# Kernel optimization log

Hardware: AMD Instinct MI355X
Metric: run time of the kernel (lower is better)

## Reference

```python
import jax, jax.numpy as jnp
import numpy as np

D = 256
H = 8
HD = D // H
LN_EPS = 1e-5


def setup_inputs() -> dict:
    key = jax.random.key(0)
    ks = jax.random.split(key, 20)
    N = 768
    s = lambda *sh: 1.0 / np.sqrt(sh[-1])
    inp = {
        "features": jax.random.normal(ks[0], (N, D), jnp.float32),
        "boxes": jax.random.uniform(ks[1], (N, 4), jnp.float32),
        # MultiheadAttention params (torch layout: [out, in])
        "in_proj_w": jax.random.normal(ks[2], (3 * D, D), jnp.float32) * s(D),
        "in_proj_b": jnp.zeros((3 * D,), jnp.float32),
        "out_proj_w": jax.random.normal(ks[3], (D, D), jnp.float32) * s(D),
        "out_proj_b": jnp.zeros((D,), jnp.float32),
        # similarity_net params
        "w1": jax.random.normal(ks[4], (256, 3 * D + 3), jnp.float32) * s(3 * D + 3),
        "b1": jnp.zeros((256,), jnp.float32),
        "ln_g": jnp.ones((256,), jnp.float32),
        "ln_b": jnp.zeros((256,), jnp.float32),
        "w2": jax.random.normal(ks[5], (128, 256), jnp.float32) * s(256),
        "b2": jnp.zeros((128,), jnp.float32),
        "w3": jax.random.normal(ks[6], (64, 128), jnp.float32) * s(128),
        "b3": jnp.zeros((64,), jnp.float32),
        "w4": jax.random.normal(ks[7], (32, 64), jnp.float32) * s(64),
        "b4": jnp.zeros((32,), jnp.float32),
        "w5": jax.random.normal(ks[8], (1, 32), jnp.float32) * s(32),
        "b5": jnp.zeros((1,), jnp.float32),
    }
    return inp


def _mha(x, in_w, in_b, out_w, out_b):
    # x: [N, D]; torch nn.MultiheadAttention self-attention (eval mode)
    N = x.shape[0]
    qkv = x @ in_w.T + in_b                      # [N, 3D]
    q, k, v = jnp.split(qkv, 3, axis=-1)
    q = q.reshape(N, H, HD).transpose(1, 0, 2)   # [H, N, HD]
    k = k.reshape(N, H, HD).transpose(1, 0, 2)
    v = v.reshape(N, H, HD).transpose(1, 0, 2)
    scores = jnp.einsum("hnd,hmd->hnm", q, k) / np.sqrt(HD)
    attn = jax.nn.softmax(scores, axis=-1)
    o = jnp.einsum("hnm,hmd->hnd", attn, v)      # [H, N, HD]
    o = o.transpose(1, 0, 2).reshape(N, D)
    return o @ out_w.T + out_b


def reference(features, boxes, in_proj_w, in_proj_b, out_proj_w, out_proj_b,
              w1, b1, ln_g, ln_b, w2, b2, w3, b3, w4, b4, w5, b5):
    N = features.shape[0]
    att = _mha(features, in_proj_w, in_proj_b, out_proj_w, out_proj_b)  # [N, D]

    fi = jnp.broadcast_to(att[:, None, :], (N, N, D))
    fj = jnp.broadcast_to(att[None, :, :], (N, N, D))
    bi = boxes[:, None, :]
    bj = boxes[None, :, :]
    x_dist = jnp.abs(bi[:, :, 0] - bj[:, :, 0])
    y_diff = bi[:, :, 1] - bj[:, :, 1]
    spatial = jnp.stack([x_dist, jnp.abs(y_diff), y_diff], axis=-1)    # [N, N, 3]
    pairs = jnp.concatenate([fi, fj, fi * fj, spatial], axis=-1)       # [N, N, 3D+3]

    h = jax.nn.relu(pairs @ w1.T + b1)
    mu = jnp.mean(h, axis=-1, keepdims=True)
    var = jnp.var(h, axis=-1, keepdims=True)
    h = (h - mu) / jnp.sqrt(var + LN_EPS) * ln_g + ln_b
    h = jax.nn.relu(h @ w2.T + b2)
    h = jax.nn.relu(h @ w3.T + b3)
    h = jax.nn.relu(h @ w4.T + b4)
    logits = (h @ w5.T + b5)[..., 0]                                   # [N, N]

    eye = jnp.eye(N, dtype=logits.dtype)
    return logits * (1.0 - eye) - 1e9 * eye
```

## Files before the change

### kernel.cpp

```cpp
#include <hip/hip_runtime.h>


typedef __attribute__((ext_vector_type(8))) __bf16 bf16x8;
typedef __attribute__((ext_vector_type(4))) float f32x4;
typedef __attribute__((ext_vector_type(8))) int i32x8;

__device__ __forceinline__ float bf2f(unsigned short u) {
    return __uint_as_float(((unsigned int)u) << 16);
}
__device__ __forceinline__ unsigned short f2bf(float f) {
    union { __bf16 b; unsigned short u; } cv;
    cv.b = (__bf16)f;
    return cv.u;
}
__device__ __forceinline__ unsigned pk2(float lo, float hi) {
    return (unsigned)f2bf(lo) | ((unsigned)f2bf(hi) << 16);
}
__device__ __forceinline__ int pk4_fp8(float a, float b, float c, float d) {
    int w = __builtin_amdgcn_cvt_pk_fp8_f32(a, b, 0, false);
    w = __builtin_amdgcn_cvt_pk_fp8_f32(c, d, w, true);
    return w;
}
__device__ __forceinline__ unsigned char f2fp8(float v) {
    return (unsigned char)(__builtin_amdgcn_cvt_pk_fp8_f32(v, 0.f, 0, false) & 0xff);
}
__device__ __forceinline__ bf16x8 load8f_bf(const float* p) {
    float4 a = *reinterpret_cast<const float4*>(p);
    float4 b = *reinterpret_cast<const float4*>(p + 4);
    union { bf16x8 v; unsigned u[4]; } cv;
    cv.u[0] = pk2(a.x, a.y); cv.u[1] = pk2(a.z, a.w);
    cv.u[2] = pk2(b.x, b.y); cv.u[3] = pk2(b.z, b.w);
    return cv.v;
}
__device__ __forceinline__ i32x8 ld32_lds(const unsigned char* p) {
    union { i32x8 v; uint4 q[2]; } r;
    r.q[0] = *reinterpret_cast<const uint4*>(p);
    r.q[1] = *reinterpret_cast<const uint4*>(p + 16);
    return r.v;
}
#define SC1 0x7F7F7F7F
#define MFMA_MX(a, b, c) __builtin_amdgcn_mfma_scale_f32_16x16x128_f8f6f4( \
        (a), (b), (c), 0, 0, 0, SC1, 0, SC1)

__global__ __launch_bounds__(256) void pack_all(
    const float* __restrict__ features, const float* __restrict__ in_proj_w,
    const float* __restrict__ in_proj_b, const float* __restrict__ out_proj_w,
    const float* __restrict__ w1, const float* __restrict__ w2,
    const float* __restrict__ w3, const float* __restrict__ w4,
    const float* __restrict__ b1, const float* __restrict__ ln_g,
    const float* __restrict__ ln_b, const float* __restrict__ b2,
    const float* __restrict__ out_proj_b,
    unsigned short* __restrict__ qkvb, unsigned short* __restrict__ Vt,
    unsigned short* __restrict__ WcatB,
    unsigned char* __restrict__ w1c_mx, unsigned char* __restrict__ w1t_f8,
    unsigned char* __restrict__ w2g_mx, unsigned char* __restrict__ w3_mx,
    unsigned char* __restrict__ w4_f8,
    float* __restrict__ bias768, float* __restrict__ c1, float* __restrict__ c2)
{
    const int blk = blockIdx.x;
    if (blk < 716) {
        int t = blk * 256 + threadIdx.x;
        if (t < 65536) {
            WcatB[t] = f2bf(out_proj_w[t]);
        } else if (t < 131072) {
            int u = t - 65536;
            int e = u & 31, lane = (u >> 5) & 63, f = u >> 11;
            int mt = f & 15, ks = f >> 4;
            int o = mt * 16 + (lane & 15);
            int k = ks * 128 + ((lane >> 4) & 3) * 32 + e;
            w1c_mx[u] = f2fp8(w1[o * 771 + 512 + k]);
        } else if (t < 139264) {
            int u = t - 131072;
            int e = u & 7, lane = (u >> 3) & 63, f = u >> 9;
            int o = f * 16 + (lane & 15);
            int k = ((lane >> 4) & 3) * 8 + e;
            float v = (k < 3) ? w1[o * 771 + 768 + k] : 0.f;
            w1t_f8[u] = f2fp8(v);
        } else if (t < 172032) {
            int u = t - 139264;
            int e = u & 31, lane = (u >> 5) & 63, f = u >> 11;
            int mt = f & 7, ks = f >> 3;
            int p = mt * 16 + (lane & 15);
            int k = ks * 128 + ((lane >> 4) & 3) * 32 + e;
            w2g_mx[u] = f2fp8(w2[p * 256 + k] * ln_g[k]);
        } else if (t < 180224) {
            int u = t - 172032;
            int e = u & 31, lane = (u >> 5) & 63, f = u >> 11;
            int o = f * 16 + (lane & 15);
            int k = ((lane >> 4) & 3) * 32 + e;
            w3_mx[u] = f2fp8(w3[o * 128 + k]);
        } else if (t < 182272) {
            int u = t - 180224;
            int e = u & 7, lane = (u >> 3) & 63, f = u >> 9;
            int l15 = lane & 15, quad = lane >> 4;
            int ct = f & 1, kc = f >> 1;
            int o = ct * 16 + l15, k = kc * 32 + quad * 8 + e;
            w4_f8[u] = f2fp8(w4[o * 64 + k]);
        } else if (t < 183040) {
            int n = t - 182272;
            if (n < 256) bias768[n] = out_proj_b[n];
            else {
                int m = n - 256;
                float s = 0.f;
                for (int d = 0; d < 256; d += 4) {
                    float4 ob = *reinterpret_cast<const float4*>(&out_proj_b[d]);
                    const float* wr = (m < 256) ? &w1[m * 771 + d]
                                                : &w1[(m - 256) * 771 + 256 + d];
                    float4 w = *reinterpret_cast<const float4*>(wr);
                    s += ob.x * w.x + ob.y * w.y + ob.z * w.z + ob.w * w.w;
                }
                bias768[n] = s + ((m < 256) ? b1[m] : 0.f);
            }
        } else if (t < 183168) {
            int p = t - 183040;
            float s2 = 0.f, s1 = 0.f;
            for (int k = 0; k < 256; k += 4) {
                float4 w = *reinterpret_cast<const float4*>(&w2[p * 256 + k]);
                float4 g = *reinterpret_cast<const float4*>(&ln_g[k]);
                float4 lb = *reinterpret_cast<const float4*>(&ln_b[k]);
                s2 += g.x * w.x + g.y * w.y + g.z * w.z + g.w * w.w;
                s1 += lb.x * w.x + lb.y * w.y + lb.z * w.z + lb.w * w.w;
            }
            c2[p] = s2;
            c1[p] = s1 + b2[p];
        }
    } else if (blk < 1228) {
        const int n = blk - 716, e = threadIdx.x;
        const float* wrow = (n < 256) ? &w1[n * 771] : &w1[(n - 256) * 771 + 256];
        float acc = 0.f;
        for (int d = 0; d < 256; d += 4) {
            float4 w = *reinterpret_cast<const float4*>(&wrow[d]);
            acc += w.x * out_proj_w[(d + 0) * 256 + e];
            acc += w.y * out_proj_w[(d + 1) * 256 + e];
            acc += w.z * out_proj_w[(d + 2) * 256 + e];
            acc += w.w * out_proj_w[(d + 3) * 256 + e];
        }
        WcatB[(256 + n) * 256 + e] = f2bf(acc);
    } else {
        const int q = blk - 1228;
        const int bm = q % 12, bn = q / 12;
        const int wv = threadIdx.x >> 6, lane = threadIdx.x & 63;
        const int l15 = lane & 15, quad = lane >> 4;
        const int row0 = bm * 64 + wv * 16;
        const int col0 = bn * 64;
        f32x4 acc[4] = {};
        for (int kc = 0; kc < 8; ++kc) {
            bf16x8 a = load8f_bf(&features[(row0 + l15) * 256 + kc * 32 + quad * 8]);
#pragma unroll
            for (int ct = 0; ct < 4; ++ct) {
                bf16x8 b = load8f_bf(&in_proj_w[(col0 + ct * 16 + l15) * 256 + kc * 32 + quad * 8]);
                acc[ct] = __builtin_amdgcn_mfma_f32_16x16x32_bf16(a, b, acc[ct], 0, 0, 0);
            }
        }
#pragma unroll
        for (int ct = 0; ct < 4; ++ct)
#pragma unroll
            for (int r = 0; r < 4; ++r) {
                int row = row0 + quad * 4 + r, col = col0 + ct * 16 + l15;
                float v = acc[ct][r] + in_proj_b[col];
                if (col < 512) qkvb[row * 768 + col] = f2bf(v);
                else           Vt[(col - 512) * 768 + row] = f2bf(v);
            }
    }
}

__global__ __launch_bounds__(256) void gemm_attab(
    const unsigned short* __restrict__ A, const unsigned short* __restrict__ W,
    const float* __restrict__ bias, float* __restrict__ att,
    float* __restrict__ AB)
{
    const int wv = threadIdx.x >> 6, lane = threadIdx.x & 63;
    const int l15 = lane & 15, quad = lane >> 4;
    const int row0 = blockIdx.x * 64 + wv * 16;
    const int col0 = blockIdx.y * 64;
    f32x4 acc[4] = {};
    for (int kc = 0; kc < 8; ++kc) {
        bf16x8 a = *reinterpret_cast<const bf16x8*>(&A[(row0 + l15) * 256 + kc * 32 + quad * 8]);
#pragma unroll
        for (int ct = 0; ct < 4; ++ct) {
            bf16x8 b = *reinterpret_cast<const bf16x8*>(&W[(col0 + ct * 16 + l15) * 256 + kc * 32 + quad * 8]);
            acc[ct] = __builtin_amdgcn_mfma_f32_16x16x32_bf16(a, b, acc[ct], 0, 0, 0);
        }
    }
#pragma unroll
    for (int ct = 0; ct < 4; ++ct)
#pragma unroll
        for (int r = 0; r < 4; ++r) {
            int row = row0 + quad * 4 + r, col = col0 + ct * 16 + l15;
            float v = acc[ct][r] + bias[col];
            if (col < 256) att[row * 256 + col] = v;
            else           AB[row * 512 + (col - 256)] = v;
        }
}

#define SP 776

__global__ __launch_bounds__(256) void attn_mfma(
    const unsigned short* __restrict__ qkvb, const unsigned short* __restrict__ Vt,
    unsigned short* __restrict__ Obf)
{
    __shared__ __align__(16) unsigned short smS[32 * SP];
    __shared__ float s_inv[32];
    const int h = blockIdx.x, q0 = blockIdx.y * 32, hb = h * 32;
    const int tid = threadIdx.x, wave = tid >> 6, lane = tid & 63;
    const int l15 = lane & 15, quad = lane >> 4;

    bf16x8 af[2];
#pragma unroll
    for (int mt = 0; mt < 2; ++mt)
        af[mt] = *reinterpret_cast<const bf16x8*>(&qkvb[(q0 + mt * 16 + l15) * 768 + hb + quad * 8]);
#pragma unroll
    for (int ct = 0; ct < 12; ++ct) {
        int n0 = wave * 192 + ct * 16;
        bf16x8 b = *reinterpret_cast<const bf16x8*>(&qkvb[(n0 + l15) * 768 + 256 + hb + quad * 8]);
#pragma unroll
        for (int mt = 0; mt < 2; ++mt) {
            f32x4 c = {};
            c = __builtin_amdgcn_mfma_f32_16x16x32_bf16(af[mt], b, c, 0, 0, 0);
#pragma unroll
            for (int r = 0; r < 4; ++r)
                smS[(mt * 16 + quad * 4 + r) * SP + n0 + l15] =
                    f2bf(c[r] * 0.17677669529663689f);
        }
    }
    __syncthreads();

    {
        const int row = tid >> 3, part = tid & 7;
        unsigned short* rp = &smS[row * SP + part * 96];
        float ls = 0.f;
#pragma unroll
        for (int c8 = 0; c8 < 12; ++c8) {
            uint4 v = *reinterpret_cast<const uint4*>(&rp[c8 * 8]);
            const unsigned short* pe = reinterpret_cast<const unsigned short*>(&v);
            unsigned short o8[8];
#pragma unroll
            for (int e = 0; e < 8; ++e) {
                float ev = __expf(bf2f(pe[e]));
                ls += ev;
                o8[e] = f2bf(ev);
            }
            *reinterpret_cast<uint4*>(&rp[c8 * 8]) = *reinterpret_cast<const uint4*>(o8);
        }
        ls += __shfl_xor(ls, 1, 64);
        ls += __shfl_xor(ls, 2, 64);
        ls += __shfl_xor(ls, 4, 64);
        if (part == 0) s_inv[row] = 1.0f / ls;
    }
    __syncthreads();

    const int row0 = (wave >> 1) * 16, cg = wave & 1;
    f32x4 accp = {};
    for (int kc = 0; kc < 24; ++kc) {
        bf16x8 a = *reinterpret_cast<const bf16x8*>(&smS[(row0 + l15) * SP + kc * 32 + quad * 8]);
        bf16x8 b = *reinterpret_cast<const bf16x8*>(&Vt[(hb + cg * 16 + l15) * 768 + kc * 32 + quad * 8]);
        accp = __builtin_amdgcn_mfma_f32_16x16x32_bf16(a, b, accp, 0, 0, 0);
    }
#pragma unroll
    for (int r = 0; r < 4; ++r) {
        int rloc = row0 + quad * 4 + r;
        Obf[(q0 + rloc) * 256 + hb + cg * 16 + l15] = f2bf(accp[r] * s_inv[rloc]);
    }
}

#define S1 304
#define S2 144
#define S3 72

__global__ __launch_bounds__(256, 4) void pair_mlp(
    const float* __restrict__ att, const float* __restrict__ AB,
    const unsigned char* __restrict__ w1c_mx, const unsigned char* __restrict__ w1t_f8,
    const unsigned char* __restrict__ w2g_mx, const unsigned char* __restrict__ w3_mx,
    const unsigned char* __restrict__ w4_f8,
    const float* __restrict__ boxes,
    const float* __restrict__ c1, const float* __restrict__ c2,
    const float* __restrict__ b3, const float* __restrict__ b4,
    const float* __restrict__ w5, const float* __restrict__ b5,
    float* __restrict__ out)
{
    __shared__ __align__(16) unsigned char smH[64 * S1];
    __shared__ __align__(16) unsigned char smH2[64 * S2];
    __shared__ __align__(16) unsigned char smH3[64 * S3];
    __shared__ float s_psum[64][4], s_pssq[64][4];
    __shared__ float s_mu[64], s_rs[64];
    __shared__ float s_l5[64][2];

    const int i    = blockIdx.x;
    const int j0   = blockIdx.y * 64;
    const int tid  = threadIdx.x;
    const int wave = tid >> 6;
    const int lane = tid & 63;
    const int l15  = lane & 15;
    const int quad = lane >> 4;

    {
        const int g = tid & 63;
        float4 fi4 = *reinterpret_cast<const float4*>(&att[i * 256 + g * 4]);
#pragma unroll 4
        for (int it = 0; it < 16; ++it) {
            int r = (tid >> 6) + it * 4;
            float4 aj = *reinterpret_cast<const float4*>(&att[(j0 + r) * 256 + g * 4]);
            *reinterpret_cast<int*>(&smH[r * S1 + g * 4]) =
                pk4_fp8(aj.x * fi4.x, aj.y * fi4.y, aj.z * fi4.z, aj.w * fi4.w);
        }
    }
    if (tid < 64) {
        int j = j0 + tid;
        float xd = fabsf(boxes[i * 4 + 0] - boxes[j * 4 + 0]);
        float yd = boxes[i * 4 + 1] - boxes[j * 4 + 1];
        *reinterpret_cast<int*>(&smH[tid * S1 + 256]) = pk4_fp8(xd, fabsf(yd), yd, 0.f);
        *reinterpret_cast<int*>(&smH[tid * S1 + 260]) = 0;
        *reinterpret_cast<long long*>(&smH[tid * S1 + 264]) = 0;
        *reinterpret_cast<long long*>(&smH[tid * S1 + 272]) = 0;
        *reinterpret_cast<long long*>(&smH[tid * S1 + 280]) = 0;
    }
    __syncthreads();

    f32x4 acc1[4][4] = {};
#pragma unroll
    for (int ks = 0; ks < 2; ++ks) {
#pragma unroll
        for (int mh = 0; mh < 2; ++mh) {
            i32x8 a0 = *reinterpret_cast<const i32x8*>(&w1c_mx[((ks * 16 + wave * 4 + mh * 2 + 0) * 64 + lane) * 32]);
            i32x8 a1 = *reinterpret_cast<const i32x8*>(&w1c_mx[((ks * 16 + wave * 4 + mh * 2 + 1) * 64 + lane) * 32]);
#pragma unroll
            for (int nt = 0; nt < 4; ++nt) {
                i32x8 b = ld32_lds(&smH[(nt * 16 + l15) * S1 + ks * 128 + quad * 32]);
                acc1[mh * 2 + 0][nt] = MFMA_MX(a0, b, acc1[mh * 2 + 0][nt]);
                acc1[mh * 2 + 1][nt] = MFMA_MX(a1, b, acc1[mh * 2 + 1][nt]);
            }
        }
    }
    {
#pragma unroll
        for (int mh = 0; mh < 2; ++mh) {
            long long a0 = *reinterpret_cast<const long long*>(&w1t_f8[((wave * 4 + mh * 2 + 0) * 64 + lane) * 8]);
            long long a1 = *reinterpret_cast<const long long*>(&w1t_f8[((wave * 4 + mh * 2 + 1) * 64 + lane) * 8]);
#pragma unroll
            for (int nt = 0; nt < 4; ++nt) {
                long long b = *reinterpret_cast<const long long*>(&smH[(nt * 16 + l15) * S1 + 256 + quad * 8]);
                acc1[mh * 2 + 0][nt] = __builtin_amdgcn_mfma_f32_16x16x32_fp8_fp8(a0, b, acc1[mh * 2 + 0][nt], 0, 0, 0);
                acc1[mh * 2 + 1][nt] = __builtin_amdgcn_mfma_f32_16x16x32_fp8_fp8(a1, b, acc1[mh * 2 + 1][nt], 0, 0, 0);
            }
        }
    }

    const int o0 = wave * 64;
    float vsum[4] = {}, vssq[4] = {};
#pragma unroll
    for (int mt = 0; mt < 4; ++mt) {
        int o = o0 + mt * 16 + quad * 4;
        float4 Ai = *reinterpret_cast<const float4*>(&AB[i * 512 + o]);
        float AiA[4] = {Ai.x, Ai.y, Ai.z, Ai.w};
#pragma unroll
        for (int nt = 0; nt < 4; ++nt) {
            int j = nt * 16 + l15;
            float4 Bj = *reinterpret_cast<const float4*>(&AB[(j0 + j) * 512 + 256 + o]);
            float BjA[4] = {Bj.x, Bj.y, Bj.z, Bj.w};
#pragma unroll
            for (int r = 0; r < 4; ++r) {
                float v = fmaxf(acc1[mt][nt][r] + AiA[r] + BjA[r], 0.f);
                acc1[mt][nt][r] = v;
                vsum[nt] += v; vssq[nt] += v * v;
            }
        }
    }
#pragma unroll
    for (int nt = 0; nt < 4; ++nt) {
        vsum[nt] += __shfl_xor(vsum[nt], 16, 64);
        vsum[nt] += __shfl_xor(vsum[nt], 32, 64);
        vssq[nt] += __shfl_xor(vssq[nt], 16, 64);
        vssq[nt] += __shfl_xor(vssq[nt], 32, 64);
    }
    if (quad == 0)
#pragma unroll
        for (int nt = 0; nt < 4; ++nt) {
            s_psum[nt * 16 + l15][wave] = vsum[nt];
            s_pssq[nt * 16 + l15][wave] = vssq[nt];
        }
    __syncthreads();
#pragma unroll
    for (int mt = 0; mt < 4; ++mt) {
        int o = o0 + mt * 16 + quad * 4;
#pragma unroll
        for (int nt = 0; nt < 4; ++nt) {
            int j = nt * 16 + l15;
            *reinterpret_cast<int*>(&smH[j * S1 + o]) =
                pk4_fp8(acc1[mt][nt][0], acc1[mt][nt][1], acc1[mt][nt][2], acc1[mt][nt][3]);
        }
    }
    if (wave == 0) {
        int j = lane;
        float sm = (s_psum[j][0] + s_psum[j][1] + s_psum[j][2] + s_psum[j][3]) * (1.0f / 256.0f);
        float sq = (s_pssq[j][0] + s_pssq[j][1] + s_pssq[j][2] + s_pssq[j][3]) * (1.0f / 256.0f);
        s_mu[j] = sm;
        s_rs[j] = rsqrtf(sq - sm * sm + 1e-5f);
    }
    __syncthreads();

    f32x4 acc2[2][4] = {};
#pragma unroll
    for (int ks = 0; ks < 2; ++ks) {
        i32x8 a0 = *reinterpret_cast<const i32x8*>(&w2g_mx[((ks * 8 + wave * 2 + 0) * 64 + lane) * 32]);
        i32x8 a1 = *reinterpret_cast<const i32x8*>(&w2g_mx[((ks * 8 + wave * 2 + 1) * 64 + lane) * 32]);
#pragma unroll
        for (int nt = 0; nt < 4; ++nt) {
            i32x8 b = ld32_lds(&smH[(nt * 16 + l15) * S1 + ks * 128 + quad * 32]);
            acc2[0][nt] = MFMA_MX(a0, b, acc2[0][nt]);
            acc2[1][nt] = MFMA_MX(a1, b, acc2[1][nt]);
        }
    }
#pragma unroll
    for (int mt = 0; mt < 2; ++mt) {
        int p = wave * 32 + mt * 16 + quad * 4;
        float4 C1 = *reinterpret_cast<const float4*>(&c1[p]);
        float4 C2 = *reinterpret_cast<const float4*>(&c2[p]);
        float C1A[4] = {C1.x, C1.y, C1.z, C1.w};
        float C2A[4] = {C2.x, C2.y, C2.z, C2.w};
#pragma unroll
        for (int nt = 0; nt < 4; ++nt) {
            int j = nt * 16 + l15;
            float mu = s_mu[j], rs = s_rs[j];
            float vv[4];
#pragma unroll
            for (int r = 0; r < 4; ++r)
                vv[r] = fmaxf(rs * (acc2[mt][nt][r] - mu * C2A[r]) + C1A[r], 0.f);
            *reinterpret_cast<int*>(&smH2[j * S2 + p]) = pk4_fp8(vv[0], vv[1], vv[2], vv[3]);
        }
    }
    __syncthreads();

    f32x4 acc3[4] = {};
    {
        i32x8 a = *reinterpret_cast<const i32x8*>(&w3_mx[(wave * 64 + lane) * 32]);
#pragma unroll
        for (int nt = 0; nt < 4; ++nt) {
            i32x8 b = ld32_lds(&smH2[(nt * 16 + l15) * S2 + quad * 32]);
            acc3[nt] = MFMA_MX(a, b, acc3[nt]);
        }
    }
    {
        int q = wave * 16 + quad * 4;
        float4 B3 = *reinterpret_cast<const float4*>(&b3[q]);
        float B3A[4] = {B3.x, B3.y, B3.z, B3.w};
#pragma unroll
        for (int nt = 0; nt < 4; ++nt) {
            int j = nt * 16 + l15;
            float vv[4];
#pragma unroll
            for (int r = 0; r < 4; ++r)
                vv[r] = fmaxf(acc3[nt][r] + B3A[r], 0.f);
            *reinterpret_cast<int*>(&smH3[j * S3 + q]) = pk4_fp8(vv[0], vv[1], vv[2], vv[3]);
        }
    }
    __syncthreads();

    const int mt4 = wave & 1;
    const int jh  = wave >> 1;
    f32x4 acc4[2] = {};
#pragma unroll
    for (int kc = 0; kc < 2; ++kc) {
        long long a = *reinterpret_cast<const long long*>(&w4_f8[((kc * 2 + mt4) * 64 + lane) * 8]);
#pragma unroll
        for (int nt = 0; nt < 2; ++nt) {
            int j = jh * 32 + nt * 16 + l15;
            long long b = *reinterpret_cast<const long long*>(&smH3[j * S3 + kc * 32 + quad * 8]);
            acc4[nt] = __builtin_amdgcn_mfma_f32_16x16x32_fp8_fp8(a, b, acc4[nt], 0, 0, 0);
        }
    }
    {
        int o4 = mt4 * 16 + quad * 4;
        float4 B4 = *reinterpret_cast<const float4*>(&b4[o4]);
        float4 W5 = *reinterpret_cast<const float4*>(&w5[o4]);
        float B4A[4] = {B4.x, B4.y, B4.z, B4.w};
        float W5A[4] = {W5.x, W5.y, W5.z, W5.w};
#pragma unroll
        for (int nt = 0; nt < 2; ++nt) {
            float part = 0.f;
#pragma unroll
            for (int r = 0; r < 4; ++r)
                part += fmaxf(acc4[nt][r] + B4A[r], 0.f) * W5A[r];
            part += __shfl_xor(part, 16, 64);
            part += __shfl_xor(part, 32, 64);
            if (quad == 0)
                s_l5[jh * 32 + nt * 16 + l15][mt4] = part;
        }
    }
    __syncthreads();
    if (tid < 64) {
        int j = j0 + tid;
        float v = s_l5[tid][0] + s_l5[tid][1] + b5[0];
        out[i * 768 + j] = (j == i) ? -1.0e9f : v;
    }
}

extern "C" void kernel_launch(void* const* d_in, const int* in_sizes, int n_in,
                              void* d_out, int out_size, void* d_ws, size_t ws_size,
                              hipStream_t stream)
{
    const float* features   = (const float*)d_in[0];
    const float* boxes      = (const float*)d_in[1];
    const float* in_proj_w  = (const float*)d_in[2];
    const float* in_proj_b  = (const float*)d_in[3];
    const float* out_proj_w = (const float*)d_in[4];
    const float* out_proj_b = (const float*)d_in[5];
    const float* w1  = (const float*)d_in[6];
    const float* b1  = (const float*)d_in[7];
    const float* ln_g = (const float*)d_in[8];
    const float* ln_b = (const float*)d_in[9];
    const float* w2  = (const float*)d_in[10];
    const float* b2  = (const float*)d_in[11];
    const float* w3  = (const float*)d_in[12];
    const float* b3  = (const float*)d_in[13];
    const float* w4  = (const float*)d_in[14];
    const float* b4  = (const float*)d_in[15];
    const float* w5  = (const float*)d_in[16];
    const float* b5  = (const float*)d_in[17];
    float* out = (float*)d_out;

    char* p = (char*)d_ws;
    unsigned short* qkvb  = (unsigned short*)p; p += 768 * 768 * 2;
    unsigned short* Vt    = (unsigned short*)p; p += 256 * 768 * 2;
    unsigned short* Obf   = (unsigned short*)p; p += 768 * 256 * 2;
    unsigned short* WcatB = (unsigned short*)p; p += 196608 * 2;
    float* att = (float*)p; p += 768 * 256 * 4;
    float* AB  = (float*)p; p += 768 * 512 * 4;
    unsigned char* w1c_mx = (unsigned char*)p; p += 65536;
    unsigned char* w1t_f8 = (unsigned char*)p; p += 8192;
    unsigned char* w2g_mx = (unsigned char*)p; p += 32768;
    unsigned char* w3_mx  = (unsigned char*)p; p += 8192;
    unsigned char* w4_f8  = (unsigned char*)p; p += 2048;
    float* bias768 = (float*)p; p += 768 * 4;
    float* c1v     = (float*)p; p += 128 * 4;
    float* c2v     = (float*)p; p += 128 * 4;

    pack_all<<<dim3(1372), dim3(256), 0, stream>>>(features, in_proj_w,
        in_proj_b, out_proj_w, w1, w2, w3, w4, b1, ln_g, ln_b, b2, out_proj_b,
        qkvb, Vt, WcatB, w1c_mx, w1t_f8, w2g_mx, w3_mx, w4_f8,
        bias768, c1v, c2v);
    attn_mfma<<<dim3(8, 24), dim3(256), 0, stream>>>(qkvb, Vt, Obf);
    gemm_attab<<<dim3(12, 12), dim3(256), 0, stream>>>(Obf, WcatB, bias768,
        att, AB);
    pair_mlp<<<dim3(768, 12), dim3(256), 0, stream>>>(att, AB,
        w1c_mx, w1t_f8, w2g_mx, w3_mx, w4_f8, boxes, c1v, c2v,
        b3, b4, w5, b5, out);
}
```

Before: 315.8 us.

## Split pair_mlp work across 8 waves per block instead of 4

Doubles the pair_mlp block to 512 threads and repartitions every layer's MFMA tiles so each wave owns half as many output rows or columns. Layer 1 goes from 4 to 2 m-tiles per wave, layer 2 from 2 to 1, and layers 3 and 4 split over j as well. The aim is to cut per-wave accumulator registers and serial MFMA chains, giving more latency hiding within a block. The cost is lower per-wave reuse of B fragments loaded from LDS, more waves contending at each barrier, and occupancy capped by the new launch bounds.

```diff
diff --git a/kernel.cpp b/kernel.cpp
--- a/kernel.cpp
+++ b/kernel.cpp
@@ -267,7 +267,7 @@
 #define S2 144
 #define S3 72
 
-__global__ __launch_bounds__(256, 4) void pair_mlp(
+__global__ __launch_bounds__(512, 2) void pair_mlp(
     const float* __restrict__ att, const float* __restrict__ AB,
     const unsigned char* __restrict__ w1c_mx, const unsigned char* __restrict__ w1t_f8,
     const unsigned char* __restrict__ w2g_mx, const unsigned char* __restrict__ w3_mx,
@@ -281,7 +281,7 @@
     __shared__ __align__(16) unsigned char smH[64 * S1];
     __shared__ __align__(16) unsigned char smH2[64 * S2];
     __shared__ __align__(16) unsigned char smH3[64 * S3];
-    __shared__ float s_psum[64][4], s_pssq[64][4];
+    __shared__ float s_psum[64][8], s_pssq[64][8];
     __shared__ float s_mu[64], s_rs[64];
     __shared__ float s_l5[64][2];
 
@@ -297,8 +297,8 @@
         const int g = tid & 63;
         float4 fi4 = *reinterpret_cast<const float4*>(&att[i * 256 + g * 4]);
 #pragma unroll 4
-        for (int it = 0; it < 16; ++it) {
-            int r = (tid >> 6) + it * 4;
+        for (int it = 0; it < 8; ++it) {
+            int r = (tid >> 6) + it * 8;
             float4 aj = *reinterpret_cast<const float4*>(&att[(j0 + r) * 256 + g * 4]);
             *reinterpret_cast<int*>(&smH[r * S1 + g * 4]) =
                 pk4_fp8(aj.x * fi4.x, aj.y * fi4.y, aj.z * fi4.z, aj.w * fi4.w);
@@ -316,39 +316,33 @@
     }
     __syncthreads();
 
-    f32x4 acc1[4][4] = {};
+    f32x4 acc1[2][4] = {};
 #pragma unroll
     for (int ks = 0; ks < 2; ++ks) {
-#pragma unroll
-        for (int mh = 0; mh < 2; ++mh) {
-            i32x8 a0 = *reinterpret_cast<const i32x8*>(&w1c_mx[((ks * 16 + wave * 4 + mh * 2 + 0) * 64 + lane) * 32]);
-            i32x8 a1 = *reinterpret_cast<const i32x8*>(&w1c_mx[((ks * 16 + wave * 4 + mh * 2 + 1) * 64 + lane) * 32]);
-#pragma unroll
-            for (int nt = 0; nt < 4; ++nt) {
-                i32x8 b = ld32_lds(&smH[(nt * 16 + l15) * S1 + ks * 128 + quad * 32]);
-                acc1[mh * 2 + 0][nt] = MFMA_MX(a0, b, acc1[mh * 2 + 0][nt]);
-                acc1[mh * 2 + 1][nt] = MFMA_MX(a1, b, acc1[mh * 2 + 1][nt]);
-            }
-        }
-    }
-    {
-#pragma unroll
-        for (int mh = 0; mh < 2; ++mh) {
-            long long a0 = *reinterpret_cast<const long long*>(&w1t_f8[((wave * 4 + mh * 2 + 0) * 64 + lane) * 8]);
-            long long a1 = *reinterpret_cast<const long long*>(&w1t_f8[((wave * 4 + mh * 2 + 1) * 64 + lane) * 8]);
-#pragma unroll
-            for (int nt = 0; nt < 4; ++nt) {
-                long long b = *reinterpret_cast<const long long*>(&smH[(nt * 16 + l15) * S1 + 256 + quad * 8]);
-                acc1[mh * 2 + 0][nt] = __builtin_amdgcn_mfma_f32_16x16x32_fp8_fp8(a0, b, acc1[mh * 2 + 0][nt], 0, 0, 0);
-                acc1[mh * 2 + 1][nt] = __builtin_amdgcn_mfma_f32_16x16x32_fp8_fp8(a1, b, acc1[mh * 2 + 1][nt], 0, 0, 0);
-            }
-        }
-    }
-
-    const int o0 = wave * 64;
+        i32x8 a0 = *reinterpret_cast<const i32x8*>(&w1c_mx[((ks * 16 + wave * 2 + 0) * 64 + lane) * 32]);
+        i32x8 a1 = *reinterpret_cast<const i32x8*>(&w1c_mx[((ks * 16 + wave * 2 + 1) * 64 + lane) * 32]);
+#pragma unroll
+        for (int nt = 0; nt < 4; ++nt) {
+            i32x8 b = ld32_lds(&smH[(nt * 16 + l15) * S1 + ks * 128 + quad * 32]);
+            acc1[0][nt] = MFMA_MX(a0, b, acc1[0][nt]);
+            acc1[1][nt] = MFMA_MX(a1, b, acc1[1][nt]);
+        }
+    }
+    {
+        long long a0 = *reinterpret_cast<const long long*>(&w1t_f8[((wave * 2 + 0) * 64 + lane) * 8]);
+        long long a1 = *reinterpret_cast<const long long*>(&w1t_f8[((wave * 2 + 1) * 64 + lane) * 8]);
+#pragma unroll
+        for (int nt = 0; nt < 4; ++nt) {
+            long long b = *reinterpret_cast<const long long*>(&smH[(nt * 16 + l15) * S1 + 256 + quad * 8]);
+            acc1[0][nt] = __builtin_amdgcn_mfma_f32_16x16x32_fp8_fp8(a0, b, acc1[0][nt], 0, 0, 0);
+            acc1[1][nt] = __builtin_amdgcn_mfma_f32_16x16x32_fp8_fp8(a1, b, acc1[1][nt], 0, 0, 0);
+        }
+    }
+
+    const int o0 = wave * 32;
     float vsum[4] = {}, vssq[4] = {};
 #pragma unroll
-    for (int mt = 0; mt < 4; ++mt) {
+    for (int mt = 0; mt < 2; ++mt) {
         int o = o0 + mt * 16 + quad * 4;
         float4 Ai = *reinterpret_cast<const float4*>(&AB[i * 512 + o]);
         float AiA[4] = {Ai.x, Ai.y, Ai.z, Ai.w};
@@ -380,7 +374,7 @@
         }
     __syncthreads();
 #pragma unroll
-    for (int mt = 0; mt < 4; ++mt) {
+    for (int mt = 0; mt < 2; ++mt) {
         int o = o0 + mt * 16 + quad * 4;
 #pragma unroll
         for (int nt = 0; nt < 4; ++nt) {
@@ -391,28 +385,27 @@
     }
     if (wave == 0) {
         int j = lane;
-        float sm = (s_psum[j][0] + s_psum[j][1] + s_psum[j][2] + s_psum[j][3]) * (1.0f / 256.0f);
-        float sq = (s_pssq[j][0] + s_pssq[j][1] + s_pssq[j][2] + s_pssq[j][3]) * (1.0f / 256.0f);
+        float sm = 0.f, sq = 0.f;
+#pragma unroll
+        for (int w = 0; w < 8; ++w) { sm += s_psum[j][w]; sq += s_pssq[j][w]; }
+        sm *= (1.0f / 256.0f); sq *= (1.0f / 256.0f);
         s_mu[j] = sm;
         s_rs[j] = rsqrtf(sq - sm * sm + 1e-5f);
     }
     __syncthreads();
 
-    f32x4 acc2[2][4] = {};
+    f32x4 acc2[4] = {};
 #pragma unroll
     for (int ks = 0; ks < 2; ++ks) {
-        i32x8 a0 = *reinterpret_cast<const i32x8*>(&w2g_mx[((ks * 8 + wave * 2 + 0) * 64 + lane) * 32]);
-        i32x8 a1 = *reinterpret_cast<const i32x8*>(&w2g_mx[((ks * 8 + wave * 2 + 1) * 64 + lane) * 32]);
+        i32x8 a = *reinterpret_cast<const i32x8*>(&w2g_mx[((ks * 8 + wave) * 64 + lane) * 32]);
 #pragma unroll
         for (int nt = 0; nt < 4; ++nt) {
             i32x8 b = ld32_lds(&smH[(nt * 16 + l15) * S1 + ks * 128 + quad * 32]);
-            acc2[0][nt] = MFMA_MX(a0, b, acc2[0][nt]);
-            acc2[1][nt] = MFMA_MX(a1, b, acc2[1][nt]);
-        }
-    }
-#pragma unroll
-    for (int mt = 0; mt < 2; ++mt) {
-        int p = wave * 32 + mt * 16 + quad * 4;
+            acc2[nt] = MFMA_MX(a, b, acc2[nt]);
+        }
+    }
+    {
+        int p = wave * 16 + quad * 4;
         float4 C1 = *reinterpret_cast<const float4*>(&c1[p]);
         float4 C2 = *reinterpret_cast<const float4*>(&c2[p]);
         float C1A[4] = {C1.x, C1.y, C1.z, C1.w};
@@ -424,49 +417,49 @@
             float vv[4];
 #pragma unroll
             for (int r = 0; r < 4; ++r)
-                vv[r] = fmaxf(rs * (acc2[mt][nt][r] - mu * C2A[r]) + C1A[r], 0.f);
+                vv[r] = fmaxf(rs * (acc2[nt][r] - mu * C2A[r]) + C1A[r], 0.f);
             *reinterpret_cast<int*>(&smH2[j * S2 + p]) = pk4_fp8(vv[0], vv[1], vv[2], vv[3]);
         }
     }
     __syncthreads();
 
-    f32x4 acc3[4] = {};
-    {
-        i32x8 a = *reinterpret_cast<const i32x8*>(&w3_mx[(wave * 64 + lane) * 32]);
-#pragma unroll
-        for (int nt = 0; nt < 4; ++nt) {
-            i32x8 b = ld32_lds(&smH2[(nt * 16 + l15) * S2 + quad * 32]);
-            acc3[nt] = MFMA_MX(a, b, acc3[nt]);
-        }
-    }
-    {
-        int q = wave * 16 + quad * 4;
+    const int qt  = wave >> 1;
+    const int jh2 = wave & 1;
+    f32x4 acc3[2] = {};
+    {
+        i32x8 a = *reinterpret_cast<const i32x8*>(&w3_mx[(qt * 64 + lane) * 32]);
+#pragma unroll
+        for (int ntl = 0; ntl < 2; ++ntl) {
+            int j = (jh2 * 2 + ntl) * 16 + l15;
+            i32x8 b = ld32_lds(&smH2[j * S2 + quad * 32]);
+            acc3[ntl] = MFMA_MX(a, b, acc3[ntl]);
+        }
+    }
+    {
+        int q = qt * 16 + quad * 4;
         float4 B3 = *reinterpret_cast<const float4*>(&b3[q]);
         float B3A[4] = {B3.x, B3.y, B3.z, B3.w};
 #pragma unroll
-        for (int nt = 0; nt < 4; ++nt) {
-            int j = nt * 16 + l15;
+        for (int ntl = 0; ntl < 2; ++ntl) {
+            int j = (jh2 * 2 + ntl) * 16 + l15;
             float vv[4];
 #pragma unroll
             for (int r = 0; r < 4; ++r)
-                vv[r] = fmaxf(acc3[nt][r] + B3A[r], 0.f);
+                vv[r] = fmaxf(acc3[ntl][r] + B3A[r], 0.f);
             *reinterpret_cast<int*>(&smH3[j * S3 + q]) = pk4_fp8(vv[0], vv[1], vv[2], vv[3]);
         }
     }
     __syncthreads();
 
     const int mt4 = wave & 1;
-    const int jh  = wave >> 1;
-    f32x4 acc4[2] = {};
+    const int jq  = wave >> 1;
+    f32x4 acc4 = {};
 #pragma unroll
     for (int kc = 0; kc < 2; ++kc) {
         long long a = *reinterpret_cast<const long long*>(&w4_f8[((kc * 2 + mt4) * 64 + lane) * 8]);
-#pragma unroll
-        for (int nt = 0; nt < 2; ++nt) {
-            int j = jh * 32 + nt * 16 + l15;
-            long long b = *reinterpret_cast<const long long*>(&smH3[j * S3 + kc * 32 + quad * 8]);
-            acc4[nt] = __builtin_amdgcn_mfma_f32_16x16x32_fp8_fp8(a, b, acc4[nt], 0, 0, 0);
-        }
+        int j = jq * 16 + l15;
+        long long b = *reinterpret_cast<const long long*>(&smH3[j * S3 + kc * 32 + quad * 8]);
+        acc4 = __builtin_amdgcn_mfma_f32_16x16x32_fp8_fp8(a, b, acc4, 0, 0, 0);
     }
     {
         int o4 = mt4 * 16 + quad * 4;
@@ -474,17 +467,14 @@
         float4 W5 = *reinterpret_cast<const float4*>(&w5[o4]);
         float B4A[4] = {B4.x, B4.y, B4.z, B4.w};
         float W5A[4] = {W5.x, W5.y, W5.z, W5.w};
-#pragma unroll
-        for (int nt = 0; nt < 2; ++nt) {
-            float part = 0.f;
-#pragma unroll
-            for (int r = 0; r < 4; ++r)
-                part += fmaxf(acc4[nt][r] + B4A[r], 0.f) * W5A[r];
-            part += __shfl_xor(part, 16, 64);
-            part += __shfl_xor(part, 32, 64);
-            if (quad == 0)
-                s_l5[jh * 32 + nt * 16 + l15][mt4] = part;
-        }
+        float part = 0.f;
+#pragma unroll
+        for (int r = 0; r < 4; ++r)
+            part += fmaxf(acc4[r] + B4A[r], 0.f) * W5A[r];
+        part += __shfl_xor(part, 16, 64);
+        part += __shfl_xor(part, 32, 64);
+        if (quad == 0)
+            s_l5[jq * 16 + l15][mt4] = part;
     }
     __syncthreads();
     if (tid < 64) {
@@ -541,7 +531,7 @@
     attn_mfma<<<dim3(8, 24), dim3(256), 0, stream>>>(qkvb, Vt, Obf);
     gemm_attab<<<dim3(12, 12), dim3(256), 0, stream>>>(Obf, WcatB, bias768,
         att, AB);
-    pair_mlp<<<dim3(768, 12), dim3(256), 0, stream>>>(att, AB,
+    pair_mlp<<<dim3(768, 12), dim3(512), 0, stream>>>(att, AB,
         w1c_mx, w1t_f8, w2g_mx, w3_mx, w4_f8, boxes, c1v, c2v,
         b3, b4, w5, b5, out);
 }
```

Result: faster. 297.0 us (-6.0%).
